# Kernel tuning notes

Measured on AMD Instinct MI355X. Metric: run time of the kernel, lower is better.

## Reference

```python
import jax, jax.numpy as jnp
import numpy as np

EMBED_DIM = 1024
NUM_HEADS = 16
HEAD_DIM = EMBED_DIM // NUM_HEADS
T, B = 2048, 2


def setup_inputs() -> dict:
    key = jax.random.key(0)
    ks = jax.random.split(key, 12)
    s = 1.0 / np.sqrt(EMBED_DIM)
    x = jax.random.normal(ks[0], (T, B, EMBED_DIM), dtype=jnp.float32)
    time_decay = jax.random.uniform(ks[1], (T, B, 1), dtype=jnp.float32)
    # causal mask: masked_fill where mask == 0
    attn_mask = jnp.tril(jnp.ones((T, T), dtype=jnp.int32))
    Wq = jax.random.uniform(ks[2], (EMBED_DIM, EMBED_DIM), jnp.float32, -s, s)
    bq = jax.random.uniform(ks[3], (EMBED_DIM,), jnp.float32, -s, s)
    Wk = jax.random.uniform(ks[4], (EMBED_DIM, EMBED_DIM), jnp.float32, -s, s)
    bk = jax.random.uniform(ks[5], (EMBED_DIM,), jnp.float32, -s, s)
    Wv = jax.random.uniform(ks[6], (EMBED_DIM, EMBED_DIM), jnp.float32, -s, s)
    bv = jax.random.uniform(ks[7], (EMBED_DIM,), jnp.float32, -s, s)
    Wo = jax.random.uniform(ks[8], (EMBED_DIM, EMBED_DIM), jnp.float32, -s, s)
    bo = jax.random.uniform(ks[9], (EMBED_DIM,), jnp.float32, -s, s)
    return {"x": x, "time_decay": time_decay, "attn_mask": attn_mask,
            "Wq": Wq, "bq": bq, "Wk": Wk, "bk": bk,
            "Wv": Wv, "bv": bv, "Wo": Wo, "bo": bo}


def reference(x, time_decay, attn_mask, Wq, bq, Wk, bk, Wv, bv, Wo, bo):
    t, b, e = x.shape
    h, d = NUM_HEADS, HEAD_DIM
    # linear (torch: y = x @ W.T + b), then split heads -> (B, H, T, D)
    def proj(W, bias):
        y = jnp.einsum('tbe,fe->tbf', x, W) + bias
        return y.reshape(t, b, h, d).transpose(1, 2, 0, 3)
    Q, K, V = proj(Wq, bq), proj(Wk, bk), proj(Wv, bv)
    scores = jnp.einsum('bhqd,bhkd->bhqk', Q, K) / np.sqrt(d).astype(jnp.float32)
    scores = jnp.where(attn_mask == 0, jnp.float32(-1e9), scores)
    attn = jax.nn.softmax(scores, axis=-1)
    out = jnp.einsum('bhqk,bhkd->bhqd', attn, V)      # (B,H,T,D)
    out = out.transpose(2, 0, 1, 3).reshape(t, b, e)   # (T,B,E)
    out = jnp.einsum('tbe,fe->tbf', out, Wo) + bo
    return out * time_decay
```

## Files before the change

### kernel.cpp

```cpp
#include <hip/hip_runtime.h>


typedef unsigned short u16;
typedef unsigned int u32;
typedef __attribute__((ext_vector_type(8))) short bf16x8_t;
typedef __attribute__((ext_vector_type(4))) float fx4_t;

#define T_SEQ 2048
#define BATCH 2
#define EMB   1024
#define NH    16
#define HD    64
#define MROWS (T_SEQ * BATCH)

#define EXP2F(x) __builtin_amdgcn_exp2f(x)

__device__ __forceinline__ float bf2f(u16 u) {
  union { unsigned int i; float f; } v;
  v.i = ((unsigned int)u) << 16;
  return v.f;
}
__device__ __forceinline__ u16 f2bf(float f) {
  union { float f; unsigned int i; } v;
  v.f = f;
  unsigned int x = v.i;
  unsigned int r = (x + 0x7fffu + ((x >> 16) & 1u)) >> 16;
  return (u16)r;
}
__device__ __forceinline__ u32 fbits(float f) {
  union { float f; u32 i; } v; v.f = f; return v.i;
}

__device__ __forceinline__ void glds16(const void* g, void* l) {
  __builtin_amdgcn_global_load_lds(
      (const __attribute__((address_space(1))) unsigned int*)g,
      (__attribute__((address_space(3))) unsigned int*)l, 16, 0, 0);
}


__global__ void cvt_all(const float* __restrict__ x,
                        const float* __restrict__ wq, const float* __restrict__ wk,
                        const float* __restrict__ wv, const float* __restrict__ wo,
                        u16* __restrict__ xb,
                        u16* __restrict__ wqb, u16* __restrict__ wkb,
                        u16* __restrict__ wvb, u16* __restrict__ wob) {
  int i = blockIdx.x * blockDim.x + threadIdx.x;
  const float* src; u16* dst; int off;
  if (i < 1048576)      { src = x;  dst = xb;  off = i; }
  else if (i < 1310720) { src = wq; dst = wqb; off = i - 1048576; }
  else if (i < 1572864) { src = wk; dst = wkb; off = i - 1310720; }
  else if (i < 1835008) { src = wv; dst = wvb; off = i - 1572864; }
  else                  { src = wo; dst = wob; off = i - 1835008; }
  float4 v = ((const float4*)src)[off];
  ushort4 o;
  o.x = f2bf(v.x); o.y = f2bf(v.y); o.z = f2bf(v.z); o.w = f2bf(v.w);
  ((ushort4*)dst)[off] = o;
}

__global__ __launch_bounds__(256, 3) void gemm_qkv(
    const u16* __restrict__ xb,
    const u16* __restrict__ wq, const u16* __restrict__ wk, const u16* __restrict__ wv,
    const float* __restrict__ bq, const float* __restrict__ bk, const float* __restrict__ bv,
    u16* __restrict__ Qm, u16* __restrict__ Km, u16* __restrict__ VTg) {
  __shared__ short As[2][128 * 64];
  __shared__ short Bs[2][64 * 64];

  const int z = blockIdx.z;
  const u16* W = (z == 0) ? wq : (z == 1) ? wk : wv;
  const float* bias = (z == 0) ? bq : (z == 1) ? bk : bv;

  const int tid = threadIdx.x;
  const int bm = blockIdx.x, bn = blockIdx.y;
  const int lane = tid & 63, w = tid >> 6;
  const int wm = w >> 1, wn = w & 1;
  const int lr = lane & 15, quad = lane >> 4;
  const int r0 = lane >> 3;
  const int c8s = ((lane & 7) ^ r0) * 8;
  const int sw = (lr & 7);

  fx4_t acc[4][2];
#pragma unroll
  for (int i = 0; i < 4; i++)
#pragma unroll
    for (int j = 0; j < 2; j++) acc[i][j] = (fx4_t){0.f, 0.f, 0.f, 0.f};

#define STAGE(kt_, bi_)                                                          \
  {                                                                              \
    const int k0_ = (kt_) * 64;                                                  \
    _Pragma("unroll")                                                            \
    for (int i = 0; i < 4; i++) {             \
      const int rr = w * 32 + i * 8;                                             \
      const int ml = bm * 128 + rr + r0;                                         \
      const int grow = (z == 2) ? (((ml & 2047) << 1) | (ml >> 11)) : ml;        \
      glds16(xb + (size_t)grow * EMB + k0_ + c8s, &As[bi_][rr * 64]);            \
    }                                                                            \
    _Pragma("unroll")                                                            \
    for (int i = 0; i < 2; i++) {              \
      const int rr = w * 16 + i * 8;                                             \
      glds16(W + (size_t)(bn * 64 + rr + r0) * EMB + k0_ + c8s,                  \
             &Bs[bi_][rr * 64]);                                                 \
    }                                                                            \
  }

  const int nkt = EMB / 64;
  STAGE(0, 0);
  __syncthreads();

  for (int kt = 0; kt < nkt; kt++) {
    const int buf = kt & 1;
    if (kt + 1 < nkt) STAGE(kt + 1, buf ^ 1);
#pragma unroll
    for (int ks = 0; ks < 2; ++ks) {
      bf16x8_t a[4], b[2];
#pragma unroll
      for (int i = 0; i < 4; i++)
        a[i] = *(const bf16x8_t*)&As[buf][(wm * 64 + i * 16 + lr) * 64 + (((ks * 4 + quad) ^ sw) * 8)];
#pragma unroll
      for (int j = 0; j < 2; j++)
        b[j] = *(const bf16x8_t*)&Bs[buf][(wn * 32 + j * 16 + lr) * 64 + (((ks * 4 + quad) ^ sw) * 8)];
      if (z == 2) {
#pragma unroll
        for (int i = 0; i < 4; i++)
#pragma unroll
          for (int j = 0; j < 2; j++)
            acc[i][j] = __builtin_amdgcn_mfma_f32_16x16x32_bf16(b[j], a[i], acc[i][j], 0, 0, 0);
      } else {
#pragma unroll
        for (int i = 0; i < 4; i++)
#pragma unroll
          for (int j = 0; j < 2; j++)
            acc[i][j] = __builtin_amdgcn_mfma_f32_16x16x32_bf16(a[i], b[j], acc[i][j], 0, 0, 0);
      }
    }
    __syncthreads();
  }
#undef STAGE

  if (z == 2) {
#pragma unroll
    for (int i = 0; i < 4; i++) {
#pragma unroll
      for (int j = 0; j < 2; j++) {
#pragma unroll
        for (int r = 0; r < 4; r++) {
          const int n = bn * 64 + wn * 32 + j * 16 + quad * 4 + r;
          const int ml = bm * 128 + wm * 64 + i * 16 + lr;
          const int t = ml & 2047, bb = ml >> 11;
          const int h = n >> 6, d = n & 63;
          VTg[((size_t)(bb * NH + h) * HD + d) * T_SEQ + t] = f2bf(acc[i][j][r] + bias[n]);
        }
      }
    }
  } else {
    u16* dst = (z == 0) ? Qm : Km;
#pragma unroll
    for (int i = 0; i < 4; i++) {
#pragma unroll
      for (int j = 0; j < 2; j++) {
        const int n = bn * 64 + wn * 32 + j * 16 + lr;
        const float bsv = bias[n];
#pragma unroll
        for (int r = 0; r < 4; r++) {
          const int m = bm * 128 + wm * 64 + i * 16 + quad * 4 + r;
          dst[(size_t)m * EMB + n] = f2bf(acc[i][j][r] + bsv);
        }
      }
    }
  }
}

__global__ __launch_bounds__(256, 2) void gemm_out(
    const u16* __restrict__ Ob, const u16* __restrict__ wo,
    const float* __restrict__ bo, const float* __restrict__ td,
    float* __restrict__ out) {
  __shared__ short As[64 * 64];
  __shared__ short Bs[128 * 64];

  const int tid = threadIdx.x;
  const int bm = blockIdx.x, bn = blockIdx.y;
  const int lane = tid & 63, w = tid >> 6;
  const int wm = w >> 1, wn = w & 1;
  const int lr = lane & 15, quad = lane >> 4;
  const int r0 = lane >> 3;
  const int c8s = ((lane & 7) ^ r0) * 8;
  const int sw = (lr & 7);

  fx4_t acc[2][4];
#pragma unroll
  for (int i = 0; i < 2; i++)
#pragma unroll
    for (int j = 0; j < 4; j++) acc[i][j] = (fx4_t){0.f, 0.f, 0.f, 0.f};

  for (int k0 = 0; k0 < EMB; k0 += 64) {
#pragma unroll
    for (int i = 0; i < 2; i++) {
      const int rr = w * 16 + i * 8;
      glds16(Ob + (size_t)(bm * 64 + rr + r0) * EMB + k0 + c8s, &As[rr * 64]);
    }
#pragma unroll
    for (int i = 0; i < 4; i++) {
      const int rr = w * 32 + i * 8;
      glds16(wo + (size_t)(bn * 128 + rr + r0) * EMB + k0 + c8s, &Bs[rr * 64]);
    }
    __syncthreads();
#pragma unroll
    for (int ks = 0; ks < 2; ++ks) {
      bf16x8_t a[2], b[4];
#pragma unroll
      for (int i = 0; i < 2; i++)
        a[i] = *(const bf16x8_t*)&As[(wm * 32 + i * 16 + lr) * 64 + (((ks * 4 + quad) ^ sw) * 8)];
#pragma unroll
      for (int j = 0; j < 4; j++)
        b[j] = *(const bf16x8_t*)&Bs[(wn * 64 + j * 16 + lr) * 64 + (((ks * 4 + quad) ^ sw) * 8)];
#pragma unroll
      for (int i = 0; i < 2; i++)
#pragma unroll
        for (int j = 0; j < 4; j++)
          acc[i][j] = __builtin_amdgcn_mfma_f32_16x16x32_bf16(a[i], b[j], acc[i][j], 0, 0, 0);
    }
    __syncthreads();
  }

#pragma unroll
  for (int i = 0; i < 2; i++) {
#pragma unroll
    for (int j = 0; j < 4; j++) {
      const int n = bn * 128 + wn * 64 + j * 16 + lr;
      const float bsv = bo[n];
#pragma unroll
      for (int r = 0; r < 4; r++) {
        const int m = bm * 64 + wm * 32 + i * 16 + quad * 4 + r;
        out[(size_t)m * EMB + n] = (acc[i][j][r] + bsv) * td[m];
      }
    }
  }
}

__global__ __launch_bounds__(256, 4) void attn_mfma8(
    const u16* __restrict__ Qm, const u16* __restrict__ Km, const u16* __restrict__ VTg,
    u16* __restrict__ Ob) {
  __shared__ short Kd[2][64 * 64];
  __shared__ short Vd[2][64 * 64];
  __shared__ short Ps[4][16 * 64];

  const int blk = blockIdx.x;
  const int bh = blk & 31;
  const int j = blk >> 5;
  const int qt = (j & 1) ? (31 - (j >> 1)) : (j >> 1);
  const int qb = qt * 64;
  const int b = bh >> 4, h = bh & 15;

  const int tid = threadIdx.x;
  const int w = tid >> 6, lane = tid & 63;
  const int lr = lane & 15, quad = lane >> 4;
  const int r0 = lane >> 3;
  const int c8s = ((lane & 7) ^ r0) * 8;
  const int sw = (lr & 7);
  const int pkey = (lr & 7) << 1;

  const u16* Qbase = Qm + (size_t)b * EMB + (size_t)h * HD;
  const u16* Kbase = Km + (size_t)b * EMB + (size_t)h * HD;
  const u16* VTb = VTg + (size_t)bh * HD * T_SEQ;

  const float QSCALE = 0.18033688f;
  bf16x8_t qf[2];
#pragma unroll
  for (int ks = 0; ks < 2; ks++) {
    bf16x8_t v = *(const bf16x8_t*)(Qbase + (size_t)(qb + w * 16 + lr) * 2 * EMB + ks * 32 + quad * 8);
    bf16x8_t o;
#pragma unroll
    for (int e = 0; e < 8; e++) o[e] = (short)f2bf(bf2f((u16)v[e]) * QSCALE);
    qf[ks] = o;
  }

  fx4_t acc_o[4];
#pragma unroll
  for (int dn = 0; dn < 4; dn++) acc_o[dn] = (fx4_t){0.f, 0.f, 0.f, 0.f};
  float l_par = 0.f;

#define STAGE(kt_, buf_)                                                            \
  {                                                                                 \
    const int k0_ = (kt_) * 64;                                                     \
    _Pragma("unroll")                                                               \
    for (int i = 0; i < 2; i++) {                                                   \
      const int rr = w * 16 + i * 8;                                                \
      glds16(Kbase + (size_t)(k0_ + rr + r0) * 2 * EMB + c8s, &Kd[buf_][rr * 64]);  \
      glds16(VTb + (size_t)(rr + r0) * T_SEQ + k0_ + c8s, &Vd[buf_][rr * 64]);      \
    }                                                                               \
  }

  const int nkt = qt + 1;
  STAGE(0, 0);
  __syncthreads();

  for (int kt = 0; kt < nkt; kt++) {
    const int buf = kt & 1;
    if (kt + 1 < nkt) STAGE(kt + 1, buf ^ 1);

    fx4_t st[4];
#pragma unroll
    for (int nt = 0; nt < 4; nt++) st[nt] = (fx4_t){0.f, 0.f, 0.f, 0.f};
#pragma unroll
    for (int ks = 0; ks < 2; ks++) {
#pragma unroll
      for (int nt = 0; nt < 4; nt++) {
        bf16x8_t kf = *(const bf16x8_t*)&Kd[buf][(nt * 16 + lr) * 64 + (((ks * 4 + quad) ^ sw) * 8)];
        st[nt] = __builtin_amdgcn_mfma_f32_16x16x32_bf16(kf, qf[ks], st[nt], 0, 0, 0);
      }
    }

    bf16x8_t vf[2][4];
#pragma unroll
    for (int ks = 0; ks < 2; ks++)
#pragma unroll
      for (int dn = 0; dn < 4; dn++)
        vf[ks][dn] = *(const bf16x8_t*)&Vd[buf][(dn * 16 + lr) * 64 + (((ks * 4 + quad) ^ sw) * 8)];

    if (kt == qt) {
#pragma unroll
      for (int nt = 0; nt < 4; nt++)
#pragma unroll
        for (int r = 0; r < 4; r++)
          if (nt * 16 + quad * 4 + r > w * 16 + lr) st[nt][r] = -1e30f;
    }

    short* Pw = Ps[w];
#pragma unroll
    for (int nt = 0; nt < 4; nt++) {
      float e0 = EXP2F(st[nt][0]);
      float e1 = EXP2F(st[nt][1]);
      float e2 = EXP2F(st[nt][2]);
      float e3 = EXP2F(st[nt][3]);
      u32 p01 = (fbits(e0) >> 16) | (fbits(e1) & 0xFFFF0000u);
      u32 p23 = (fbits(e2) >> 16) | (fbits(e3) & 0xFFFF0000u);
      uint2 pv; pv.x = p01; pv.y = p23;
      *(uint2*)&Pw[lr * 64 + ((nt * 4 + quad) ^ pkey) * 4] = pv;
      l_par += (e0 + e1) + (e2 + e3);
    }

#pragma unroll
    for (int ks = 0; ks < 2; ks++) {
      bf16x8_t pf = *(const bf16x8_t*)&Pw[lr * 64 + ((ks * 8 + quad * 2) ^ pkey) * 4];
#pragma unroll
      for (int dn = 0; dn < 4; dn++)
        acc_o[dn] = __builtin_amdgcn_mfma_f32_16x16x32_bf16(pf, vf[ks][dn], acc_o[dn], 0, 0, 0);
    }

    __syncthreads();
  }
#undef STAGE

  l_par += __shfl_xor(l_par, 16);
  l_par += __shfl_xor(l_par, 32);
  const float inv = 1.0f / l_par;
#pragma unroll
  for (int r = 0; r < 4; r++) {
    const float inv_r = __shfl(inv, quad * 4 + r);
    const int t = qb + w * 16 + quad * 4 + r;
#pragma unroll
    for (int dn = 0; dn < 4; dn++) {
      const int d = dn * 16 + lr;
      Ob[(size_t)(t * BATCH + b) * EMB + h * HD + d] = f2bf(acc_o[dn][r] * inv_r);
    }
  }
}

extern "C" void kernel_launch(void* const* d_in, const int* in_sizes, int n_in,
                              void* d_out, int out_size, void* d_ws, size_t ws_size,
                              hipStream_t stream) {
  const float* x  = (const float*)d_in[0];
  const float* td = (const float*)d_in[1];
  const float* Wq = (const float*)d_in[3];
  const float* bq = (const float*)d_in[4];
  const float* Wk = (const float*)d_in[5];
  const float* bk = (const float*)d_in[6];
  const float* Wv = (const float*)d_in[7];
  const float* bv = (const float*)d_in[8];
  const float* Wo = (const float*)d_in[9];
  const float* bo = (const float*)d_in[10];
  float* out = (float*)d_out;

  char* ws = (char*)d_ws;
  u16* xb  = (u16*)(ws + 0);
  u16* wqb = (u16*)(ws + ((size_t)8  << 20));
  u16* wkb = (u16*)(ws + ((size_t)10 << 20));
  u16* wvb = (u16*)(ws + ((size_t)12 << 20));
  u16* wob = (u16*)(ws + ((size_t)14 << 20));
  u16* Qm  = (u16*)(ws + ((size_t)16 << 20));
  u16* Km  = (u16*)(ws + ((size_t)24 << 20));
  u16* VTg = (u16*)(ws + ((size_t)32 << 20));
  u16* Ob  = xb;

  cvt_all<<<8192, 256, 0, stream>>>(x, Wq, Wk, Wv, Wo, xb, wqb, wkb, wvb, wob);

  gemm_qkv<<<dim3(MROWS / 128, EMB / 64, 3), 256, 0, stream>>>(
      xb, wqb, wkb, wvb, bq, bk, bv, Qm, Km, VTg);

  attn_mfma8<<<1024, 256, 0, stream>>>(Qm, Km, VTg, Ob);

  gemm_out<<<dim3(MROWS / 64, EMB / 128), 256, 0, stream>>>(Ob, wob, bo, td, out);
}
```

Measured before the change: 191.4 us.

## Load K and V fragments directly from global memory, dropping LDS staging

New measurement: 337.3 us. 76.2% more time.

```diff
diff --git a/kernel.cpp b/kernel.cpp
--- a/kernel.cpp
+++ b/kernel.cpp
@@ -236,12 +236,10 @@
   }
 }
 
-__global__ __launch_bounds__(256, 4) void attn_mfma8(
+__global__ __launch_bounds__(256, 4) void attn_gdir(
     const u16* __restrict__ Qm, const u16* __restrict__ Km, const u16* __restrict__ VTg,
     u16* __restrict__ Ob) {
-  __shared__ short Kd[2][64 * 64];
-  __shared__ short Vd[2][64 * 64];
-  __shared__ short Ps[4][16 * 64];
+  __shared__ short Ps[4][16 * 72];
 
   const int blk = blockIdx.x;
   const int bh = blk & 31;
@@ -253,15 +251,14 @@
   const int tid = threadIdx.x;
   const int w = tid >> 6, lane = tid & 63;
   const int lr = lane & 15, quad = lane >> 4;
-  const int r0 = lane >> 3;
-  const int c8s = ((lane & 7) ^ r0) * 8;
-  const int sw = (lr & 7);
-  const int pkey = (lr & 7) << 1;
 
   const u16* Qbase = Qm + (size_t)b * EMB + (size_t)h * HD;
   const u16* Kbase = Km + (size_t)b * EMB + (size_t)h * HD;
   const u16* VTb = VTg + (size_t)bh * HD * T_SEQ;
 
+  const u16* Kl = Kbase + (size_t)lr * 2 * EMB + quad * 8;
+  const u16* Vl = VTb + (size_t)lr * T_SEQ + quad * 8;
+
   const float QSCALE = 0.18033688f;
   bf16x8_t qf[2];
 #pragma unroll
@@ -278,24 +275,9 @@
   for (int dn = 0; dn < 4; dn++) acc_o[dn] = (fx4_t){0.f, 0.f, 0.f, 0.f};
   float l_par = 0.f;
 
-#define STAGE(kt_, buf_)                                                            \
-  {                                                                                 \
-    const int k0_ = (kt_) * 64;                                                     \
-    _Pragma("unroll")                                                               \
-    for (int i = 0; i < 2; i++) {                                                   \
-      const int rr = w * 16 + i * 8;                                                \
-      glds16(Kbase + (size_t)(k0_ + rr + r0) * 2 * EMB + c8s, &Kd[buf_][rr * 64]);  \
-      glds16(VTb + (size_t)(rr + r0) * T_SEQ + k0_ + c8s, &Vd[buf_][rr * 64]);      \
-    }                                                                               \
-  }
-
   const int nkt = qt + 1;
-  STAGE(0, 0);
-  __syncthreads();
-
   for (int kt = 0; kt < nkt; kt++) {
-    const int buf = kt & 1;
-    if (kt + 1 < nkt) STAGE(kt + 1, buf ^ 1);
+    const int k0 = kt * 64;
 
     fx4_t st[4];
 #pragma unroll
@@ -304,7 +286,7 @@
     for (int ks = 0; ks < 2; ks++) {
 #pragma unroll
       for (int nt = 0; nt < 4; nt++) {
-        bf16x8_t kf = *(const bf16x8_t*)&Kd[buf][(nt * 16 + lr) * 64 + (((ks * 4 + quad) ^ sw) * 8)];
+        bf16x8_t kf = *(const bf16x8_t*)(Kl + (size_t)(k0 + nt * 16) * 2 * EMB + ks * 32);
         st[nt] = __builtin_amdgcn_mfma_f32_16x16x32_bf16(kf, qf[ks], st[nt], 0, 0, 0);
       }
     }
@@ -314,7 +296,7 @@
     for (int ks = 0; ks < 2; ks++)
 #pragma unroll
       for (int dn = 0; dn < 4; dn++)
-        vf[ks][dn] = *(const bf16x8_t*)&Vd[buf][(dn * 16 + lr) * 64 + (((ks * 4 + quad) ^ sw) * 8)];
+        vf[ks][dn] = *(const bf16x8_t*)(Vl + (size_t)(dn * 16) * T_SEQ + k0 + ks * 32);
 
     if (kt == qt) {
 #pragma unroll
@@ -334,21 +316,18 @@
       u32 p01 = (fbits(e0) >> 16) | (fbits(e1) & 0xFFFF0000u);
       u32 p23 = (fbits(e2) >> 16) | (fbits(e3) & 0xFFFF0000u);
       uint2 pv; pv.x = p01; pv.y = p23;
-      *(uint2*)&Pw[lr * 64 + ((nt * 4 + quad) ^ pkey) * 4] = pv;
+      *(uint2*)&Pw[lr * 72 + nt * 16 + quad * 4] = pv;
       l_par += (e0 + e1) + (e2 + e3);
     }
 
 #pragma unroll
     for (int ks = 0; ks < 2; ks++) {
-      bf16x8_t pf = *(const bf16x8_t*)&Pw[lr * 64 + ((ks * 8 + quad * 2) ^ pkey) * 4];
+      bf16x8_t pf = *(const bf16x8_t*)&Pw[lr * 72 + ks * 32 + quad * 8];
 #pragma unroll
       for (int dn = 0; dn < 4; dn++)
         acc_o[dn] = __builtin_amdgcn_mfma_f32_16x16x32_bf16(pf, vf[ks][dn], acc_o[dn], 0, 0, 0);
     }
-
-    __syncthreads();
-  }
-#undef STAGE
+  }
 
   l_par += __shfl_xor(l_par, 16);
   l_par += __shfl_xor(l_par, 32);
@@ -396,7 +375,7 @@
   gemm_qkv<<<dim3(MROWS / 128, EMB / 64, 3), 256, 0, stream>>>(
       xb, wqb, wkb, wvb, bq, bk, bv, Qm, Km, VTg);
 
-  attn_mfma8<<<1024, 256, 0, stream>>>(Qm, Km, VTg, Ob);
+  attn_gdir<<<1024, 256, 0, stream>>>(Qm, Km, VTg, Ob);
 
   gemm_out<<<dim3(MROWS / 64, EMB / 128), 256, 0, stream>>>(Ob, wob, bo, td, out);
 }
```

## Pair causal query tiles per block and triple-buffer K/V loads in attention

Applied to the files above, without the earlier changes.

New measurement: 190.2 us. Within noise of the previous version (-0.6%).

```diff
diff --git a/kernel.cpp b/kernel.cpp
--- a/kernel.cpp
+++ b/kernel.cpp
@@ -236,18 +236,16 @@
   }
 }
 
-__global__ __launch_bounds__(256, 4) void attn_mfma8(
+__global__ __launch_bounds__(256, 2) void attn_bal(
     const u16* __restrict__ Qm, const u16* __restrict__ Km, const u16* __restrict__ VTg,
     u16* __restrict__ Ob) {
-  __shared__ short Kd[2][64 * 64];
-  __shared__ short Vd[2][64 * 64];
-  __shared__ short Ps[4][16 * 64];
+  __shared__ short Kd[3][64 * 64];
+  __shared__ short Vd[3][64 * 64];
+  __shared__ short Ps[4][16 * 72];
 
   const int blk = blockIdx.x;
   const int bh = blk & 31;
-  const int j = blk >> 5;
-  const int qt = (j & 1) ? (31 - (j >> 1)) : (j >> 1);
-  const int qb = qt * 64;
+  const int p = blk >> 5;
   const int b = bh >> 4, h = bh & 15;
 
   const int tid = threadIdx.x;
@@ -256,27 +254,12 @@
   const int r0 = lane >> 3;
   const int c8s = ((lane & 7) ^ r0) * 8;
   const int sw = (lr & 7);
-  const int pkey = (lr & 7) << 1;
 
   const u16* Qbase = Qm + (size_t)b * EMB + (size_t)h * HD;
   const u16* Kbase = Km + (size_t)b * EMB + (size_t)h * HD;
   const u16* VTb = VTg + (size_t)bh * HD * T_SEQ;
 
   const float QSCALE = 0.18033688f;
-  bf16x8_t qf[2];
-#pragma unroll
-  for (int ks = 0; ks < 2; ks++) {
-    bf16x8_t v = *(const bf16x8_t*)(Qbase + (size_t)(qb + w * 16 + lr) * 2 * EMB + ks * 32 + quad * 8);
-    bf16x8_t o;
-#pragma unroll
-    for (int e = 0; e < 8; e++) o[e] = (short)f2bf(bf2f((u16)v[e]) * QSCALE);
-    qf[ks] = o;
-  }
-
-  fx4_t acc_o[4];
-#pragma unroll
-  for (int dn = 0; dn < 4; dn++) acc_o[dn] = (fx4_t){0.f, 0.f, 0.f, 0.f};
-  float l_par = 0.f;
 
 #define STAGE(kt_, buf_)                                                            \
   {                                                                                 \
@@ -288,81 +271,111 @@
       glds16(VTb + (size_t)(rr + r0) * T_SEQ + k0_ + c8s, &Vd[buf_][rr * 64]);      \
     }                                                                               \
   }
-
-  const int nkt = qt + 1;
-  STAGE(0, 0);
-  __syncthreads();
-
-  for (int kt = 0; kt < nkt; kt++) {
-    const int buf = kt & 1;
-    if (kt + 1 < nkt) STAGE(kt + 1, buf ^ 1);
-
-    fx4_t st[4];
-#pragma unroll
-    for (int nt = 0; nt < 4; nt++) st[nt] = (fx4_t){0.f, 0.f, 0.f, 0.f};
+#define WAIT4()  asm volatile("s_waitcnt vmcnt(4)" ::: "memory")
+#define WAIT0()  asm volatile("s_waitcnt vmcnt(0)" ::: "memory")
+#define BAR()    asm volatile("s_barrier" ::: "memory")
+
+  for (int job = 0; job < 2; ++job) {
+    const int qt = job ? (31 - p) : p;
+    const int qb = qt * 64;
+
+    bf16x8_t qf[2];
 #pragma unroll
     for (int ks = 0; ks < 2; ks++) {
+      bf16x8_t v = *(const bf16x8_t*)(Qbase + (size_t)(qb + w * 16 + lr) * 2 * EMB + ks * 32 + quad * 8);
+      bf16x8_t o;
+#pragma unroll
+      for (int e = 0; e < 8; e++) o[e] = (short)f2bf(bf2f((u16)v[e]) * QSCALE);
+      qf[ks] = o;
+    }
+
+    fx4_t acc_o[4];
+#pragma unroll
+    for (int dn = 0; dn < 4; dn++) acc_o[dn] = (fx4_t){0.f, 0.f, 0.f, 0.f};
+    float l_par = 0.f;
+
+    const int nkt = qt + 1;
+    STAGE(0, 0);
+    if (nkt > 1) { STAGE(1, 1); WAIT4(); } else { WAIT0(); }
+    BAR();
+
+    for (int kt = 0; kt < nkt; kt++) {
+      const int buf = kt % 3;
+      if (kt + 2 < nkt) STAGE(kt + 2, (kt + 2) % 3);
+
+      fx4_t st[4];
+#pragma unroll
+      for (int nt = 0; nt < 4; nt++) st[nt] = (fx4_t){0.f, 0.f, 0.f, 0.f};
+#pragma unroll
+      for (int ks = 0; ks < 2; ks++) {
+#pragma unroll
+        for (int nt = 0; nt < 4; nt++) {
+          bf16x8_t kf = *(const bf16x8_t*)&Kd[buf][(nt * 16 + lr) * 64 + (((ks * 4 + quad) ^ sw) * 8)];
+          st[nt] = __builtin_amdgcn_mfma_f32_16x16x32_bf16(kf, qf[ks], st[nt], 0, 0, 0);
+        }
+      }
+
+      bf16x8_t vf[2][4];
+#pragma unroll
+      for (int ks = 0; ks < 2; ks++)
+#pragma unroll
+        for (int dn = 0; dn < 4; dn++)
+          vf[ks][dn] = *(const bf16x8_t*)&Vd[buf][(dn * 16 + lr) * 64 + (((ks * 4 + quad) ^ sw) * 8)];
+
+      if (kt == qt) {
+#pragma unroll
+        for (int nt = 0; nt < 4; nt++)
+#pragma unroll
+          for (int r = 0; r < 4; r++)
+            if (nt * 16 + quad * 4 + r > w * 16 + lr) st[nt][r] = -1e30f;
+      }
+
+      short* Pw = Ps[w];
 #pragma unroll
       for (int nt = 0; nt < 4; nt++) {
-        bf16x8_t kf = *(const bf16x8_t*)&Kd[buf][(nt * 16 + lr) * 64 + (((ks * 4 + quad) ^ sw) * 8)];
-        st[nt] = __builtin_amdgcn_mfma_f32_16x16x32_bf16(kf, qf[ks], st[nt], 0, 0, 0);
-      }
-    }
-
-    bf16x8_t vf[2][4];
-#pragma unroll
-    for (int ks = 0; ks < 2; ks++)
-#pragma unroll
-      for (int dn = 0; dn < 4; dn++)
-        vf[ks][dn] = *(const bf16x8_t*)&Vd[buf][(dn * 16 + lr) * 64 + (((ks * 4 + quad) ^ sw) * 8)];
-
-    if (kt == qt) {
-#pragma unroll
-      for (int nt = 0; nt < 4; nt++)
-#pragma unroll
-        for (int r = 0; r < 4; r++)
-          if (nt * 16 + quad * 4 + r > w * 16 + lr) st[nt][r] = -1e30f;
-    }
-
-    short* Pw = Ps[w];
-#pragma unroll
-    for (int nt = 0; nt < 4; nt++) {
-      float e0 = EXP2F(st[nt][0]);
-      float e1 = EXP2F(st[nt][1]);
-      float e2 = EXP2F(st[nt][2]);
-      float e3 = EXP2F(st[nt][3]);
-      u32 p01 = (fbits(e0) >> 16) | (fbits(e1) & 0xFFFF0000u);
-      u32 p23 = (fbits(e2) >> 16) | (fbits(e3) & 0xFFFF0000u);
-      uint2 pv; pv.x = p01; pv.y = p23;
-      *(uint2*)&Pw[lr * 64 + ((nt * 4 + quad) ^ pkey) * 4] = pv;
-      l_par += (e0 + e1) + (e2 + e3);
-    }
-
-#pragma unroll
-    for (int ks = 0; ks < 2; ks++) {
-      bf16x8_t pf = *(const bf16x8_t*)&Pw[lr * 64 + ((ks * 8 + quad * 2) ^ pkey) * 4];
-#pragma unroll
-      for (int dn = 0; dn < 4; dn++)
-        acc_o[dn] = __builtin_amdgcn_mfma_f32_16x16x32_bf16(pf, vf[ks][dn], acc_o[dn], 0, 0, 0);
+        float e0 = EXP2F(st[nt][0]);
+        float e1 = EXP2F(st[nt][1]);
+        float e2 = EXP2F(st[nt][2]);
+        float e3 = EXP2F(st[nt][3]);
+        u32 p01 = (fbits(e0) >> 16) | (fbits(e1) & 0xFFFF0000u);
+        u32 p23 = (fbits(e2) >> 16) | (fbits(e3) & 0xFFFF0000u);
+        uint2 pv; pv.x = p01; pv.y = p23;
+        *(uint2*)&Pw[lr * 72 + nt * 16 + quad * 4] = pv;
+        l_par += (e0 + e1) + (e2 + e3);
+      }
+
+#pragma unroll
+      for (int ks = 0; ks < 2; ks++) {
+        bf16x8_t pf = *(const bf16x8_t*)&Pw[lr * 72 + ks * 32 + quad * 8];
+#pragma unroll
+        for (int dn = 0; dn < 4; dn++)
+          acc_o[dn] = __builtin_amdgcn_mfma_f32_16x16x32_bf16(pf, vf[ks][dn], acc_o[dn], 0, 0, 0);
+      }
+
+      if (kt + 2 < nkt)      { WAIT4(); BAR(); }
+      else if (kt + 1 < nkt) { WAIT0(); BAR(); }
+    }
+
+    l_par += __shfl_xor(l_par, 16);
+    l_par += __shfl_xor(l_par, 32);
+    const float inv = 1.0f / l_par;
+#pragma unroll
+    for (int r = 0; r < 4; r++) {
+      const float inv_r = __shfl(inv, quad * 4 + r);
+      const int t = qb + w * 16 + quad * 4 + r;
+#pragma unroll
+      for (int dn = 0; dn < 4; dn++) {
+        const int d = dn * 16 + lr;
+        Ob[(size_t)(t * BATCH + b) * EMB + h * HD + d] = f2bf(acc_o[dn][r] * inv_r);
+      }
     }
 
     __syncthreads();
   }
 #undef STAGE
-
-  l_par += __shfl_xor(l_par, 16);
-  l_par += __shfl_xor(l_par, 32);
-  const float inv = 1.0f / l_par;
-#pragma unroll
-  for (int r = 0; r < 4; r++) {
-    const float inv_r = __shfl(inv, quad * 4 + r);
-    const int t = qb + w * 16 + quad * 4 + r;
-#pragma unroll
-    for (int dn = 0; dn < 4; dn++) {
-      const int d = dn * 16 + lr;
-      Ob[(size_t)(t * BATCH + b) * EMB + h * HD + d] = f2bf(acc_o[dn][r] * inv_r);
-    }
-  }
+#undef WAIT4
+#undef WAIT0
+#undef BAR
 }
 
 extern "C" void kernel_launch(void* const* d_in, const int* in_sizes, int n_in,
@@ -396,7 +409,7 @@
   gemm_qkv<<<dim3(MROWS / 128, EMB / 64, 3), 256, 0, stream>>>(
       xb, wqb, wkb, wvb, bq, bk, bv, Qm, Km, VTg);
 
-  attn_mfma8<<<1024, 256, 0, stream>>>(Qm, Km, VTg, Ob);
+  attn_bal<<<512, 256, 0, stream>>>(Qm, Km, VTg, Ob);
 
   gemm_out<<<dim3(MROWS / 64, EMB / 128), 256, 0, stream>>>(Ob, wob, bo, td, out);
 }
```
